# Kernel tuning notes

Hardware: AMD Instinct MI355X
Metric: run time of the kernel (lower is better)

The kernel has to match this reference:

```python
import jax, jax.numpy as jnp
import numpy as np

NUM_NODES = 50000
NUM_EDGES = 1600000
NUM_GRAPHS = 64
K_HOPS = 3


def setup_inputs() -> dict:
    key = jax.random.key(0)
    ks = jax.random.split(key, 8)
    d_in, d_h, d_out = 128, 512, 16
    x = jax.random.normal(ks[0], (NUM_NODES, d_in), dtype=jnp.float32)
    edge_index = jax.random.randint(ks[1], (2, NUM_EDGES), 0, NUM_NODES, dtype=jnp.int64)
    batch = jnp.sort(jax.random.randint(ks[2], (NUM_NODES,), 0, NUM_GRAPHS, dtype=jnp.int64))
    w1 = jax.random.normal(ks[3], (d_in, d_h), dtype=jnp.float32) / np.sqrt(d_in)
    b1 = jnp.zeros((d_h,), dtype=jnp.float32)
    w2 = jax.random.normal(ks[4], (d_h, d_h), dtype=jnp.float32) / np.sqrt(d_h)
    b2 = jnp.zeros((d_h,), dtype=jnp.float32)
    wc = jax.random.normal(ks[5], (d_h, d_out), dtype=jnp.float32) / np.sqrt(d_h)
    bc = jnp.zeros((d_out,), dtype=jnp.float32)
    return {"x": x, "edge_index": edge_index, "batch": batch,
            "w1": w1, "b1": b1, "w2": w2, "b2": b2, "wc": wc, "bc": bc}


def _propagate(x, row, col, norm):
    # one hop: out[r] += x[c] * norm  (degree-normalized scatter-add)
    msg = x[col] * norm[:, None]                      # [E+N, d]
    return jax.ops.segment_sum(msg, row, num_segments=NUM_NODES)


def reference(x, edge_index, batch, w1, b1, w2, b2, wc, bc):
    # add self loops
    loops = jnp.arange(NUM_NODES, dtype=edge_index.dtype)
    row = jnp.concatenate([edge_index[0], loops])
    col = jnp.concatenate([edge_index[1], loops])
    deg = jax.ops.segment_sum(jnp.ones_like(row, dtype=jnp.float32), row,
                              num_segments=NUM_NODES)
    deg = jnp.clip(deg, 1.0)
    norm = 1.0 / deg[row]                             # [E+N]
    # K-hop propagation (eval mode: dropout / drop_node inactive)
    h = x
    for _ in range(K_HOPS):
        h = _propagate(h, row, col, norm)
    # MLP
    h = jax.nn.relu(h @ w1 + b1)
    h = h @ w2 + b2
    # global mean pool over graphs
    sums = jax.ops.segment_sum(h, batch, num_segments=NUM_GRAPHS)
    cnts = jax.ops.segment_sum(jnp.ones((h.shape[0],), dtype=h.dtype), batch,
                               num_segments=NUM_GRAPHS)
    pooled = sums / jnp.clip(cnts, 1.0)[:, None]      # [G, d_h]
    return pooled @ wc + bc                            # [G, out]
```

## Files before the change

### kernel.cpp

```cpp
#include <hip/hip_runtime.h>
#include <hip/hip_bf16.h>
#include <hip/hip_fp8.h>

#define N_NODES 50000
#define N_EDGES 1600000
#define N_GRAPHS 64
#define D_IN 128
#define D_H 512
#define D_OUT 16

#define NBUK 391
#define BUK_CAP 4608
#define P1_EDGES 4096
#define P1_BLOCKS ((N_EDGES + P1_EDGES - 1) / P1_EDGES)

#define MSPLIT 8

typedef short bf16x8 __attribute__((ext_vector_type(8)));
typedef float f32x4 __attribute__((ext_vector_type(4)));

static __device__ __forceinline__ unsigned short f2bf(float f) {
    __hip_bfloat16 h = __float2bfloat16(f);
    return *(unsigned short*)&h;
}

static __device__ __forceinline__ float2 fp8x2_dec(unsigned short u) {
    __hip_fp8x2_e4m3 p;
    p.__x = (__hip_fp8x2_storage_t)u;
    return static_cast<float2>(p);
}

static __device__ __forceinline__ unsigned short fp8x2_enc(float a, float b) {
    __hip_fp8_e4m3 pa(a), pb(b);
    return (unsigned short)((unsigned)pa.__x | ((unsigned)pb.__x << 8));
}


__global__ __launch_bounds__(512) void partition_edges(const int* __restrict__ row,
                                                       const int* __restrict__ col,
                                                       int* __restrict__ bucket_cnt,
                                                       unsigned* __restrict__ edge_buf) {
    __shared__ unsigned recs[P1_EDGES];
    __shared__ unsigned sorted[P1_EDGES];
    __shared__ int hist4[4][NBUK];
    __shared__ int cur4[4][NBUK];
    __shared__ int gbase[NBUK];
    __shared__ int scan[512];
    int tid = threadIdx.x;
    int w2 = tid >> 7;
    int e0 = blockIdx.x * P1_EDGES;
    int m = N_EDGES - e0; if (m > P1_EDGES) m = P1_EDGES;

    for (int i = tid; i < 4 * NBUK; i += 512) ((int*)hist4)[i] = 0;
    for (int i = tid; i < 4 * NBUK; i += 512) ((int*)cur4)[i] = 0;
    __syncthreads();
    for (int i = tid; i < m; i += 512) {
        int r = row[e0 + i];
        int c = col[e0 + i];
        int buk = r >> 7;
        recs[i] = ((unsigned)buk << 23) | ((unsigned)(r & 127) << 16) | (unsigned)c;
        atomicAdd(&hist4[w2][buk], 1);
    }
    __syncthreads();
    int tot = 0;
    if (tid < NBUK) tot = hist4[0][tid] + hist4[1][tid] + hist4[2][tid] + hist4[3][tid];
    scan[tid] = (tid < NBUK) ? tot : 0;
    __syncthreads();
    for (int off = 1; off < 512; off <<= 1) {
        int v = (tid >= off) ? scan[tid - off] : 0;
        __syncthreads();
        scan[tid] += v;
        __syncthreads();
    }
    if (tid < NBUK) {
        int run = (tid == 0) ? 0 : scan[tid - 1];
        gbase[tid] = (tot > 0) ? atomicAdd(&bucket_cnt[tid], tot) : 0;
#pragma unroll
        for (int w = 0; w < 4; ++w) {
            int c = hist4[w][tid];
            hist4[w][tid] = run;
            run += c;
        }
    }
    __syncthreads();
    for (int i = tid; i < m; i += 512) {
        unsigned rec = recs[i];
        int buk = rec >> 23;
        int rank = atomicAdd(&cur4[w2][buk], 1);
        sorted[hist4[w2][buk] + rank] = rec;
    }
    __syncthreads();
    for (int p = tid; p < m; p += 512) {
        unsigned rec = sorted[p];
        int buk = rec >> 23;
        edge_buf[(size_t)buk * BUK_CAP + gbase[buk] + (p - hist4[0][buk])] = rec;
    }
}

__global__ __launch_bounds__(512) void finalize_csr(const unsigned* __restrict__ edge_buf,
                                                    const int* __restrict__ bucket_cnt,
                                                    int* __restrict__ rowptr,
                                                    float* __restrict__ invdeg,
                                                    unsigned short* __restrict__ csr_col) {
    __shared__ int hist[128], excl[128], cur[128];
    __shared__ int scan[512];
    int b = blockIdx.x;
    int tid = threadIdx.x;
    scan[tid] = (tid < NBUK) ? bucket_cnt[tid] : 0;
    __syncthreads();
    for (int off = 1; off < 512; off <<= 1) {
        int v = (tid >= off) ? scan[tid - off] : 0;
        __syncthreads();
        scan[tid] += v;
        __syncthreads();
    }
    int cnt = bucket_cnt[b];
    int base = (b == 0) ? 0 : scan[b - 1];
    const unsigned* src = edge_buf + (size_t)b * BUK_CAP;
    __syncthreads();
    if (tid < 128) { hist[tid] = 0; cur[tid] = 0; }
    __syncthreads();
    for (int i = tid; i < cnt; i += 512)
        atomicAdd(&hist[(src[i] >> 16) & 127], 1);
    __syncthreads();
    scan[tid] = (tid < 128) ? hist[tid] : 0;
    __syncthreads();
    for (int off = 1; off < 512; off <<= 1) {
        int v = (tid >= off) ? scan[tid - off] : 0;
        __syncthreads();
        scan[tid] += v;
        __syncthreads();
    }
    if (tid < 128) excl[tid] = (tid == 0) ? 0 : scan[tid - 1];
    __syncthreads();
    int r = b * 128 + tid;
    if (tid < 128 && r < N_NODES) {
        rowptr[r] = base + excl[tid];
        invdeg[r] = 1.0f / (float)(hist[tid] + 1);
    }
    if (b == NBUK - 1 && tid == 0) rowptr[N_NODES] = base + cnt;
    for (int i = tid; i < cnt; i += 512) {
        unsigned rec = src[i];
        int rl = (rec >> 16) & 127;
        int pos = excl[rl] + atomicAdd(&cur[rl], 1);
        csr_col[base + pos] = (unsigned short)(rec & 0xFFFFu);
    }
}


__global__ __launch_bounds__(256) void prep(const float* __restrict__ x,
                                            unsigned short* __restrict__ xf,
                                            const float* __restrict__ w1,
                                            unsigned short* __restrict__ w1p,
                                            const float* __restrict__ w2,
                                            const float* __restrict__ wc,
                                            const float* __restrict__ b2,
                                            const float* __restrict__ bc,
                                            const int* __restrict__ batch,
                                            float* __restrict__ wcomb,
                                            float* __restrict__ bcomb,
                                            int* __restrict__ gcnt,
                                            int* __restrict__ gstart) {
    int b = blockIdx.x;
    int tid = threadIdx.x;
    if (b < 12500) {
        int i = b * 256 + tid;
        float2 v = ((const float2*)x)[i];
        xf[i] = fp8x2_enc(v.x, v.y);
        return;
    }
    if (b < 12756) {
        int i = (b - 12500) * 256 + tid;
        int j = i & 7, lane = (i >> 3) & 63, s = (i >> 9) & 3, t = i >> 11;
        int k = s * 32 + (lane >> 4) * 8 + j;
        int n = t * 16 + (lane & 15);
        w1p[i] = f2bf(w1[(size_t)k * D_H + n]);
        return;
    }
    int fb = b - 12756;
    if (fb == 33) {
        if (tid < N_GRAPHS) {
            int g = tid;
            int lo = 0, hi = N_NODES;
            while (lo < hi) { int mid = (lo + hi) >> 1; if (batch[mid] < g) lo = mid + 1; else hi = mid; }
            int a = lo;
            lo = 0; hi = N_NODES;
            while (lo < hi) { int mid = (lo + hi) >> 1; if (batch[mid] < g + 1) lo = mid + 1; else hi = mid; }
            gcnt[g] = lo - a;
            gstart[g] = a;
            if (g == N_GRAPHS - 1) gstart[N_GRAPHS] = N_NODES;
        }
        return;
    }
    int o = tid & 15, kl = tid >> 4;
    int k = fb * 16 + kl;
    if (k > D_H) return;
    const float* wr = (k < D_H) ? (w2 + (size_t)k * D_H) : b2;
    float s = 0.f;
    for (int j = 0; j < D_H; j += 4) {
        s += wr[j + 0] * wc[(j + 0) * D_OUT + o]
           + wr[j + 1] * wc[(j + 1) * D_OUT + o]
           + wr[j + 2] * wc[(j + 2) * D_OUT + o]
           + wr[j + 3] * wc[(j + 3) * D_OUT + o];
    }
    if (k < D_H) wcomb[k * D_OUT + o] = s;
    else         bcomb[o] = s + bc[o];
}


__global__ __launch_bounds__(128) void propagate_fp8(const unsigned short* __restrict__ xin,
                                                     unsigned short* __restrict__ out8,
                                                     unsigned* __restrict__ out16,
                                                     int last, float extra,
                                                     const int* __restrict__ rowptr,
                                                     const unsigned short* __restrict__ csr_col,
                                                     const float* __restrict__ invdeg) {
    int wave = threadIdx.x >> 6;
    int lane = threadIdx.x & 63;
    int r = blockIdx.x * 2 + wave;
    if (r >= N_NODES) return;
    int beg = rowptr[r], end = rowptr[r + 1];
    float2 sv = fp8x2_dec(xin[(size_t)r * 64 + lane]);
    float acc0 = sv.x, acc1 = sv.y;
    for (int cs = beg; cs < end; cs += 64) {
        int nn = end - cs; if (nn > 64) nn = 64;
        int colv = (int)csr_col[cs + (lane < nn ? lane : 0)];
        int j = 0;
        for (; j + 16 <= nn; j += 16) {
            unsigned short uu[16];
#pragma unroll
            for (int q = 0; q < 16; ++q) {
                int c = __shfl(colv, j + q, 64);
                uu[q] = xin[(size_t)c * 64 + lane];
            }
#pragma unroll
            for (int q = 0; q < 16; ++q) {
                float2 v = fp8x2_dec(uu[q]);
                acc0 += v.x; acc1 += v.y;
            }
        }
        for (; j + 4 <= nn; j += 4) {
            unsigned short u0, u1, u2, u3;
            {
                int c0 = __shfl(colv, j + 0, 64), c1 = __shfl(colv, j + 1, 64);
                int c2 = __shfl(colv, j + 2, 64), c3 = __shfl(colv, j + 3, 64);
                u0 = xin[(size_t)c0 * 64 + lane];
                u1 = xin[(size_t)c1 * 64 + lane];
                u2 = xin[(size_t)c2 * 64 + lane];
                u3 = xin[(size_t)c3 * 64 + lane];
            }
            float2 v0 = fp8x2_dec(u0), v1 = fp8x2_dec(u1);
            float2 v2 = fp8x2_dec(u2), v3 = fp8x2_dec(u3);
            acc0 += v0.x + v1.x + v2.x + v3.x;
            acc1 += v0.y + v1.y + v2.y + v3.y;
        }
        for (; j < nn; ++j) {
            int c = __shfl(colv, j, 64);
            float2 v = fp8x2_dec(xin[(size_t)c * 64 + lane]);
            acc0 += v.x; acc1 += v.y;
        }
    }
    float s = invdeg[r] * extra;
    acc0 *= s; acc1 *= s;
    if (last) {
        out16[(size_t)r * 64 + lane] = (unsigned)f2bf(acc0) | ((unsigned)f2bf(acc1) << 16);
    } else {
        out8[(size_t)r * 64 + lane] = fp8x2_enc(acc0, acc1);
    }
}


__global__ __launch_bounds__(256) void gemm_graph_pool(const unsigned short* __restrict__ h3b,
                                                       const unsigned short* __restrict__ w1p,
                                                       const float* __restrict__ b1,
                                                       const int* __restrict__ gstart,
                                                       float* __restrict__ gsum) {
    __shared__ float wsum[4][128];
    int tid = threadIdx.x;
    int lane = tid & 63, wave = tid >> 6;
    int quad = lane >> 4, l15 = lane & 15;
    int g = blockIdx.x;
    int nbase = blockIdx.y * 128;
    int ms = blockIdx.z;
    int r0 = gstart[g], r1 = gstart[g + 1];

    float b1v[8];
#pragma unroll
    for (int t = 0; t < 8; ++t) b1v[t] = b1[nbase + t * 16 + l15];

    const unsigned short* bbase = w1p + ((size_t)(blockIdx.y * 8) * 4 * 64 + lane) * 8;

    float gaccT[8];
#pragma unroll
    for (int t = 0; t < 8; ++t) gaccT[t] = 0.f;

    for (int mbase = r0 + ms * 64; mbase < r1; mbase += 64 * MSPLIT) {
        int m = mbase + wave * 16 + l15;
        int mc = m < N_NODES ? m : N_NODES - 1;
        const unsigned short* arow = h3b + (size_t)mc * 128 + quad * 8;
        bf16x8 afrag[4];
#pragma unroll
        for (int s = 0; s < 4; ++s)
            afrag[s] = *(const bf16x8*)(arow + s * 32);

        int rowbase = mbase + wave * 16 + quad * 4;
#pragma unroll
        for (int t = 0; t < 8; ++t) {
            f32x4 acc = (f32x4){0.f, 0.f, 0.f, 0.f};
#pragma unroll
            for (int s = 0; s < 4; ++s) {
                bf16x8 bfrag = *(const bf16x8*)(bbase + (size_t)(t * 4 + s) * 64 * 8);
                acc = __builtin_amdgcn_mfma_f32_16x16x32_bf16(afrag[s], bfrag, acc, 0, 0, 0);
            }
#pragma unroll
            for (int rg = 0; rg < 4; ++rg) {
                float v = acc[rg] + b1v[t];
                v = v > 0.f ? v : 0.f;
                gaccT[t] += (rowbase + rg < r1) ? v : 0.f;
            }
        }
    }
#pragma unroll
    for (int t = 0; t < 8; ++t) {
        gaccT[t] += __shfl_xor(gaccT[t], 16, 64);
        gaccT[t] += __shfl_xor(gaccT[t], 32, 64);
    }
    if (quad == 0) {
#pragma unroll
        for (int t = 0; t < 8; ++t)
            wsum[wave][t * 16 + l15] = gaccT[t];
    }
    __syncthreads();
    if (tid < 128)
        gsum[((size_t)ms * N_GRAPHS + g) * D_H + nbase + tid] =
            wsum[0][tid] + wsum[1][tid] + wsum[2][tid] + wsum[3][tid];
}


__global__ __launch_bounds__(256) void final_pool(const float* __restrict__ gsum,
                                                  const int* __restrict__ gcnt,
                                                  const float* __restrict__ wcomb,
                                                  const float* __restrict__ bcomb,
                                                  float* __restrict__ out) {
    int g = blockIdx.x;
    int tid = threadIdx.x;
    __shared__ float p[D_H];
    __shared__ float part[16][17];
    int c = gcnt[g]; if (c < 1) c = 1;
    float inv = 1.0f / (float)c;
#pragma unroll
    for (int h = 0; h < 2; ++h) {
        int i = tid + h * 256;
        float v = 0.f;
#pragma unroll
        for (int ms = 0; ms < MSPLIT; ++ms)
            v += gsum[((size_t)ms * N_GRAPHS + g) * D_H + i];
        p[i] = v * inv;
    }
    __syncthreads();
    int o = tid & 15, ch = tid >> 4;
    int k0 = ch * 32;
    float s = 0.f;
    for (int k = k0; k < k0 + 32; ++k)
        s += p[k] * wcomb[k * D_OUT + o];
    part[ch][o] = s;
    __syncthreads();
    if (tid < D_OUT) {
        float t = bcomb[tid];
        for (int ch2 = 0; ch2 < 16; ++ch2) t += part[ch2][tid];
        out[g * D_OUT + tid] = t;
    }
}


extern "C" void kernel_launch(void* const* d_in, const int* in_sizes, int n_in,
                              void* d_out, int out_size, void* d_ws, size_t ws_size,
                              hipStream_t stream) {
    const float* x     = (const float*)d_in[0];
    const int*   eidx  = (const int*)d_in[1];
    const int*   batch = (const int*)d_in[2];
    const float* w1    = (const float*)d_in[3];
    const float* b1    = (const float*)d_in[4];
    const float* w2    = (const float*)d_in[5];
    const float* b2    = (const float*)d_in[6];
    const float* wc    = (const float*)d_in[7];
    const float* bc    = (const float*)d_in[8];
    float* out = (float*)d_out;
    const int* row = eidx;
    const int* col = eidx + N_EDGES;

    char* p = (char*)d_ws;
    auto alloc = [&](size_t bytes) { char* q = p; p += (bytes + 255) & ~(size_t)255; return q; };
    char* zbase = p;
    int*   bucket_cnt = (int*)alloc((size_t)NBUK * 4);
    size_t zbytes = (size_t)(p - zbase);
    float* gsum    = (float*)alloc((size_t)MSPLIT * N_GRAPHS * D_H * 4);
    int*   rowptr  = (int*)alloc((size_t)(N_NODES + 1) * 4);
    int*   gcnt    = (int*)alloc((size_t)N_GRAPHS * 4);
    int*   gstart  = (int*)alloc((size_t)(N_GRAPHS + 1) * 4);
    float* invdeg  = (float*)alloc((size_t)N_NODES * 4);
    float* wcomb   = (float*)alloc((size_t)D_H * D_OUT * 4);
    float* bcomb   = (float*)alloc((size_t)D_OUT * 4);
    unsigned* edge_buf = (unsigned*)alloc((size_t)NBUK * BUK_CAP * 4);
    unsigned short* csr_col = (unsigned short*)alloc((size_t)N_EDGES * 2);
    unsigned short* xf  = (unsigned short*)alloc((size_t)N_NODES * 64 * 2);
    unsigned short* h0f = (unsigned short*)alloc((size_t)N_NODES * 64 * 2);
    unsigned short* h1f = (unsigned short*)alloc((size_t)N_NODES * 64 * 2);
    unsigned* h3b  = (unsigned*)alloc((size_t)N_NODES * 64 * 4);
    unsigned short* w1p = (unsigned short*)alloc((size_t)D_IN * D_H * 2);

    (void)hipMemsetAsync(zbase, 0, zbytes, stream);

    prep<<<12790, 256, 0, stream>>>(x, xf, w1, w1p, w2, wc, b2, bc, batch,
                                    wcomb, bcomb, gcnt, gstart);

    partition_edges<<<P1_BLOCKS, 512, 0, stream>>>(row, col, bucket_cnt, edge_buf);
    finalize_csr<<<NBUK, 512, 0, stream>>>(edge_buf, bucket_cnt, rowptr, invdeg, csr_col);

    int pgrid = (N_NODES + 1) / 2;
    propagate_fp8<<<pgrid, 128, 0, stream>>>(xf,  h0f, nullptr, 0, 8.0f,
                                             rowptr, csr_col, invdeg);
    propagate_fp8<<<pgrid, 128, 0, stream>>>(h0f, h1f, nullptr, 0, 8.0f,
                                             rowptr, csr_col, invdeg);
    propagate_fp8<<<pgrid, 128, 0, stream>>>(h1f, nullptr, h3b, 1, 1.0f / 64.0f,
                                             rowptr, csr_col, invdeg);

    dim3 ggrid(N_GRAPHS, D_H / 128, MSPLIT);
    gemm_graph_pool<<<ggrid, 256, 0, stream>>>((const unsigned short*)h3b, w1p, b1,
                                               gstart, gsum);
    final_pool<<<N_GRAPHS, 256, 0, stream>>>(gsum, gcnt, wcomb, bcomb, out);
}
```

Before: 249.2 us.

## Map eight rows per wave in propagation with 16-byte vector gathers

The propagation kernel now gives each node row to an 8-lane group, so one wave handles 8 rows instead of one. Each lane gathers 16 fp8 values with a single 16-byte load instead of 2-byte loads, and column indices are prefetched one batch ahead. Out-of-range neighbours point at a zeroed padding row (index N_NODES) that prep writes into each feature buffer. This cuts load-instruction count and makes per-row work finer grained. Rows in a wave now run to the wave's maximum degree, which wastes lanes on low-degree rows.

```diff
diff --git a/kernel.cpp b/kernel.cpp
--- a/kernel.cpp
+++ b/kernel.cpp
@@ -33,6 +33,17 @@
 static __device__ __forceinline__ unsigned short fp8x2_enc(float a, float b) {
     __hip_fp8_e4m3 pa(a), pb(b);
     return (unsigned short)((unsigned)pa.__x | ((unsigned)pb.__x << 8));
+}
+
+static __device__ __forceinline__ void dec16_add(uint4 u, float* acc) {
+    unsigned vv[4] = {u.x, u.y, u.z, u.w};
+#pragma unroll
+    for (int w = 0; w < 4; ++w) {
+        float2 a = fp8x2_dec((unsigned short)(vv[w] & 0xFFFFu));
+        float2 b = fp8x2_dec((unsigned short)(vv[w] >> 16));
+        acc[w * 4 + 0] += a.x; acc[w * 4 + 1] += a.y;
+        acc[w * 4 + 2] += b.x; acc[w * 4 + 3] += b.y;
+    }
 }
 
 
@@ -160,7 +171,9 @@
                                             float* __restrict__ wcomb,
                                             float* __restrict__ bcomb,
                                             int* __restrict__ gcnt,
-                                            int* __restrict__ gstart) {
+                                            int* __restrict__ gstart,
+                                            unsigned short* __restrict__ h0f,
+                                            unsigned short* __restrict__ h1f) {
     int b = blockIdx.x;
     int tid = threadIdx.x;
     if (b < 12500) {
@@ -189,6 +202,10 @@
             gcnt[g] = lo - a;
             gstart[g] = a;
             if (g == N_GRAPHS - 1) gstart[N_GRAPHS] = N_NODES;
+        } else if (tid >= 64 && tid < 256) {
+            int t = tid - 64;
+            unsigned short* bp = (t < 64) ? xf : (t < 128 ? h0f : h1f);
+            bp[(size_t)N_NODES * 64 + (t & 63)] = 0;
         }
         return;
     }
@@ -208,64 +225,86 @@
 }
 
 
-__global__ __launch_bounds__(128) void propagate_fp8(const unsigned short* __restrict__ xin,
+__global__ __launch_bounds__(256) void propagate_fp8(const unsigned short* __restrict__ xin,
                                                      unsigned short* __restrict__ out8,
                                                      unsigned* __restrict__ out16,
                                                      int last, float extra,
                                                      const int* __restrict__ rowptr,
                                                      const unsigned short* __restrict__ csr_col,
                                                      const float* __restrict__ invdeg) {
+    int lane = threadIdx.x & 63;
     int wave = threadIdx.x >> 6;
-    int lane = threadIdx.x & 63;
-    int r = blockIdx.x * 2 + wave;
-    if (r >= N_NODES) return;
-    int beg = rowptr[r], end = rowptr[r + 1];
-    float2 sv = fp8x2_dec(xin[(size_t)r * 64 + lane]);
-    float acc0 = sv.x, acc1 = sv.y;
-    for (int cs = beg; cs < end; cs += 64) {
-        int nn = end - cs; if (nn > 64) nn = 64;
-        int colv = (int)csr_col[cs + (lane < nn ? lane : 0)];
-        int j = 0;
-        for (; j + 16 <= nn; j += 16) {
-            unsigned short uu[16];
-#pragma unroll
-            for (int q = 0; q < 16; ++q) {
-                int c = __shfl(colv, j + q, 64);
-                uu[q] = xin[(size_t)c * 64 + lane];
-            }
-#pragma unroll
-            for (int q = 0; q < 16; ++q) {
-                float2 v = fp8x2_dec(uu[q]);
-                acc0 += v.x; acc1 += v.y;
-            }
+    int l8   = lane & 7;
+    int grp  = lane >> 3;
+    int r = blockIdx.x * 32 + wave * 8 + grp;
+    bool rv = (r < N_NODES);
+    int rc = rv ? r : 0;
+    int beg = rowptr[rc];
+    int end = rowptr[rc + 1];
+    int nn = rv ? (end - beg) : 0;
+
+    int nmax = nn;
+    { int t = __shfl_xor(nmax, 8, 64);  nmax = t > nmax ? t : nmax; }
+    { int t = __shfl_xor(nmax, 16, 64); nmax = t > nmax ? t : nmax; }
+    { int t = __shfl_xor(nmax, 32, 64); nmax = t > nmax ? t : nmax; }
+
+    float acc[16];
+#pragma unroll
+    for (int i = 0; i < 16; ++i) acc[i] = 0.f;
+    {
+        uint4 u = *(const uint4*)(xin + (size_t)rc * 64 + l8 * 8);
+        dec16_add(u, acc);
+    }
+
+    int base = lane & 56;
+    int cv;
+    {
+        int jj = l8;
+        int idx = (jj < nn) ? beg + jj : 0;
+        unsigned short cl = csr_col[idx];
+        cv = (jj < nn) ? (int)cl : N_NODES;
+    }
+    for (int jb = 0; jb < nmax; jb += 8) {
+        uint4 u[8];
+#pragma unroll
+        for (int q = 0; q < 8; ++q) {
+            int c = __shfl(cv, base + q, 64);
+            u[q] = *(const uint4*)(xin + (size_t)c * 64 + l8 * 8);
         }
-        for (; j + 4 <= nn; j += 4) {
-            unsigned short u0, u1, u2, u3;
-            {
-                int c0 = __shfl(colv, j + 0, 64), c1 = __shfl(colv, j + 1, 64);
-                int c2 = __shfl(colv, j + 2, 64), c3 = __shfl(colv, j + 3, 64);
-                u0 = xin[(size_t)c0 * 64 + lane];
-                u1 = xin[(size_t)c1 * 64 + lane];
-                u2 = xin[(size_t)c2 * 64 + lane];
-                u3 = xin[(size_t)c3 * 64 + lane];
-            }
-            float2 v0 = fp8x2_dec(u0), v1 = fp8x2_dec(u1);
-            float2 v2 = fp8x2_dec(u2), v3 = fp8x2_dec(u3);
-            acc0 += v0.x + v1.x + v2.x + v3.x;
-            acc1 += v0.y + v1.y + v2.y + v3.y;
-        }
-        for (; j < nn; ++j) {
-            int c = __shfl(colv, j, 64);
-            float2 v = fp8x2_dec(xin[(size_t)c * 64 + lane]);
-            acc0 += v.x; acc1 += v.y;
-        }
-    }
-    float s = invdeg[r] * extra;
-    acc0 *= s; acc1 *= s;
+        int jn = jb + 8 + l8;
+        int idxn = (jn < nn) ? beg + jn : 0;
+        unsigned short cln = csr_col[idxn];
+        int cvn = (jn < nn) ? (int)cln : N_NODES;
+#pragma unroll
+        for (int q = 0; q < 8; ++q) dec16_add(u[q], acc);
+        cv = cvn;
+    }
+
+    float s = rv ? invdeg[r] * extra : 0.f;
+#pragma unroll
+    for (int i = 0; i < 16; ++i) acc[i] *= s;
+
+    if (!rv) return;
     if (last) {
-        out16[(size_t)r * 64 + lane] = (unsigned)f2bf(acc0) | ((unsigned)f2bf(acc1) << 16);
+        uint4 w0, w1v;
+        w0.x = (unsigned)f2bf(acc[0])  | ((unsigned)f2bf(acc[1])  << 16);
+        w0.y = (unsigned)f2bf(acc[2])  | ((unsigned)f2bf(acc[3])  << 16);
+        w0.z = (unsigned)f2bf(acc[4])  | ((unsigned)f2bf(acc[5])  << 16);
+        w0.w = (unsigned)f2bf(acc[6])  | ((unsigned)f2bf(acc[7])  << 16);
+        w1v.x = (unsigned)f2bf(acc[8])  | ((unsigned)f2bf(acc[9])  << 16);
+        w1v.y = (unsigned)f2bf(acc[10]) | ((unsigned)f2bf(acc[11]) << 16);
+        w1v.z = (unsigned)f2bf(acc[12]) | ((unsigned)f2bf(acc[13]) << 16);
+        w1v.w = (unsigned)f2bf(acc[14]) | ((unsigned)f2bf(acc[15]) << 16);
+        unsigned* dst = out16 + (size_t)r * 64 + l8 * 8;
+        *(uint4*)dst = w0;
+        *(uint4*)(dst + 4) = w1v;
     } else {
-        out8[(size_t)r * 64 + lane] = fp8x2_enc(acc0, acc1);
+        uint4 w;
+        w.x = (unsigned)fp8x2_enc(acc[0],  acc[1])  | ((unsigned)fp8x2_enc(acc[2],  acc[3])  << 16);
+        w.y = (unsigned)fp8x2_enc(acc[4],  acc[5])  | ((unsigned)fp8x2_enc(acc[6],  acc[7])  << 16);
+        w.z = (unsigned)fp8x2_enc(acc[8],  acc[9])  | ((unsigned)fp8x2_enc(acc[10], acc[11]) << 16);
+        w.w = (unsigned)fp8x2_enc(acc[12], acc[13]) | ((unsigned)fp8x2_enc(acc[14], acc[15]) << 16);
+        *(uint4*)(out8 + (size_t)r * 64 + l8 * 8) = w;
     }
 }
 
@@ -403,26 +442,26 @@
     float* bcomb   = (float*)alloc((size_t)D_OUT * 4);
     unsigned* edge_buf = (unsigned*)alloc((size_t)NBUK * BUK_CAP * 4);
     unsigned short* csr_col = (unsigned short*)alloc((size_t)N_EDGES * 2);
-    unsigned short* xf  = (unsigned short*)alloc((size_t)N_NODES * 64 * 2);
-    unsigned short* h0f = (unsigned short*)alloc((size_t)N_NODES * 64 * 2);
-    unsigned short* h1f = (unsigned short*)alloc((size_t)N_NODES * 64 * 2);
+    unsigned short* xf  = (unsigned short*)alloc((size_t)(N_NODES + 1) * 64 * 2);
+    unsigned short* h0f = (unsigned short*)alloc((size_t)(N_NODES + 1) * 64 * 2);
+    unsigned short* h1f = (unsigned short*)alloc((size_t)(N_NODES + 1) * 64 * 2);
     unsigned* h3b  = (unsigned*)alloc((size_t)N_NODES * 64 * 4);
     unsigned short* w1p = (unsigned short*)alloc((size_t)D_IN * D_H * 2);
 
     (void)hipMemsetAsync(zbase, 0, zbytes, stream);
 
     prep<<<12790, 256, 0, stream>>>(x, xf, w1, w1p, w2, wc, b2, bc, batch,
-                                    wcomb, bcomb, gcnt, gstart);
+                                    wcomb, bcomb, gcnt, gstart, h0f, h1f);
 
     partition_edges<<<P1_BLOCKS, 512, 0, stream>>>(row, col, bucket_cnt, edge_buf);
     finalize_csr<<<NBUK, 512, 0, stream>>>(edge_buf, bucket_cnt, rowptr, invdeg, csr_col);
 
-    int pgrid = (N_NODES + 1) / 2;
-    propagate_fp8<<<pgrid, 128, 0, stream>>>(xf,  h0f, nullptr, 0, 8.0f,
+    int pgrid = (N_NODES + 31) / 32;
+    propagate_fp8<<<pgrid, 256, 0, stream>>>(xf,  h0f, nullptr, 0, 8.0f,
                                              rowptr, csr_col, invdeg);
-    propagate_fp8<<<pgrid, 128, 0, stream>>>(h0f, h1f, nullptr, 0, 8.0f,
+    propagate_fp8<<<pgrid, 256, 0, stream>>>(h0f, h1f, nullptr, 0, 8.0f,
                                              rowptr, csr_col, invdeg);
-    propagate_fp8<<<pgrid, 128, 0, stream>>>(h1f, nullptr, h3b, 1, 1.0f / 64.0f,
+    propagate_fp8<<<pgrid, 256, 0, stream>>>(h1f, nullptr, h3b, 1, 1.0f / 64.0f,
                                              rowptr, csr_col, invdeg);
 
     dim3 ggrid(N_GRAPHS, D_H / 128, MSPLIT);
```

Measured after the change: 235.7 us. 5.4% less time.
